# Performance work log

Measured on AMD Instinct MI355X. Metric: run time of the kernel, lower is better.

Reference implementation:

```python
import jax, jax.numpy as jnp
import numpy as np

B, N, D, E = 2, 50000, 128, 640000


def setup_inputs() -> dict:
    key = jax.random.key(0)
    ks = jax.random.split(key, 7)
    x = jax.random.normal(ks[0], (B, N, D), dtype=jnp.float32)
    edge_index = jax.random.randint(ks[1], (2, E), 0, N)
    edge_attr = jax.random.uniform(ks[2], (E,), dtype=jnp.float32)
    s = 1.0 / np.sqrt(D)
    W1 = jax.random.uniform(ks[3], (D, D), jnp.float32, -s, s)
    b1 = jax.random.uniform(ks[4], (D,), jnp.float32, -s, s)
    W2 = jax.random.uniform(ks[5], (D, D), jnp.float32, -s, s)
    b2 = jax.random.uniform(ks[6], (D,), jnp.float32, -s, s)
    return {"x": x, "edge_index": edge_index, "edge_attr": edge_attr,
            "W1": W1, "b1": b1, "W2": W2, "b2": b2}


def _gcn_layer(x, W, b, row, col, norm, n):
    # x: [B, N, D] -> transform then gather-scale-scatter along edges
    h = jnp.einsum('bnd,df->bnf', x, W)
    msg = h[:, row, :] * norm[None, :, None]          # [B, E2, D]
    agg = jax.vmap(lambda m: jax.ops.segment_sum(m, col, num_segments=n))(msg)
    return agg + b


def reference(x, edge_index, edge_attr, W1, b1, W2, b2):
    n = x.shape[1]
    row, col = edge_index[0], edge_index[1]
    # GCNConv default: add self loops (weight 1), symmetric normalization
    loop = jnp.arange(n)
    row2 = jnp.concatenate([row, loop])
    col2 = jnp.concatenate([col, loop])
    w2 = jnp.concatenate([edge_attr, jnp.ones((n,), edge_attr.dtype)])
    deg = jax.ops.segment_sum(w2, col2, num_segments=n)
    dinv = jnp.where(deg > 0, jax.lax.rsqrt(deg), 0.0)
    norm = dinv[row2] * w2 * dinv[col2]               # [E2]
    # dropout is identity in eval mode
    h = jax.nn.relu(_gcn_layer(x, W1, b1, row2, col2, norm, n))
    h = jax.nn.relu(_gcn_layer(h, W2, b2, row2, col2, norm, n))
    return h
```

## Files before the change

### kernel.cpp

```cpp
#include <hip/hip_runtime.h>

#define NNODES 50000
#define NBATCH 2
#define DIM    128
#define NEDGE  640000
#define M_TOT  (NBATCH*NNODES)
#define NXCD   8
#define NBL_N  196

typedef unsigned short u16;
typedef unsigned int   u32;
typedef unsigned long long u64;

typedef __attribute__((ext_vector_type(8))) short bf16x8;
typedef __attribute__((ext_vector_type(4))) float f32x4;

__device__ __forceinline__ float bf2f(u16 u){ return __uint_as_float(((u32)u)<<16); }
__device__ __forceinline__ u16 f2bf(float f){
    u32 x = __float_as_uint(f);
    x += 0x7fffu + ((x>>16)&1u);
    return (u16)(x>>16);
}

__global__ __launch_bounds__(256) void count_k(const int* __restrict__ ei,
                                               const float* __restrict__ ea,
                                               u64* __restrict__ part,
                                               u32* __restrict__ rankpack){
    u32 xcc = __builtin_amdgcn_s_getreg(6164) & 7u;
    int e = blockIdx.x*256 + threadIdx.x;
    if (e < NEDGE){
        int c = ei[NEDGE + e];
        u64 inc = (((u64)__float2uint_rn(ea[e] * 16777216.0f)) << 32) | 1ull;
        u64 old = __hip_atomic_fetch_add(&part[(size_t)xcc*NNODES + c], inc,
                                         __ATOMIC_RELAXED, __HIP_MEMORY_SCOPE_WORKGROUP);
        rankpack[e] = ((u32)old & 0xffffu) | (xcc << 16);
    }
}

__global__ __launch_bounds__(256) void scan1(const u64* __restrict__ part,
                                             int* __restrict__ cnt,
                                             int* __restrict__ poff,
                                             float* __restrict__ dinv,
                                             int* colstart, int* bsum){
    __shared__ int s[256];
    int tid = threadIdx.x;
    int n = blockIdx.x*256 + tid;
    int v = 0;
    if (n < NNODES){
        int run = 0; u64 fsum = 0;
        #pragma unroll
        for (int p = 0; p < NXCD; ++p){
            u64 pv = part[(size_t)p*NNODES + n];
            poff[p*NNODES + n] = run;
            run  += (int)(pv & 0xffffffffu);
            fsum += (pv >> 32);
        }
        cnt[n] = run;
        v = run;
        float deg = 1.0f + (float)fsum * (1.0f/16777216.0f);
        dinv[n] = rsqrtf(deg);
    }
    s[tid] = v; __syncthreads();
    #pragma unroll
    for (int off = 1; off < 256; off <<= 1){
        int t = (tid >= off) ? s[tid-off] : 0;
        __syncthreads();
        s[tid] += t;
        __syncthreads();
    }
    if (n < NNODES) colstart[n] = s[tid] - v;
    if (tid == 255) bsum[blockIdx.x] = s[255];
}

__global__ __launch_bounds__(256) void scan23(int* colstart, const int* __restrict__ bsum){
    __shared__ int s[256];
    int tid = threadIdx.x;
    int v = (tid < NBL_N) ? bsum[tid] : 0;
    s[tid] = v; __syncthreads();
    #pragma unroll
    for (int off = 1; off < 256; off <<= 1){
        int t = (tid >= off) ? s[tid-off] : 0;
        __syncthreads();
        s[tid] += t;
        __syncthreads();
    }
    int add = s[blockIdx.x] - bsum[blockIdx.x];
    int i = blockIdx.x*256 + tid;
    if (i < NNODES) colstart[i] += add;
}

__global__ __launch_bounds__(256) void fill_k(const int* __restrict__ ei,
                                              const float* __restrict__ ea,
                                              const float* __restrict__ dinv,
                                              const int* __restrict__ colstart,
                                              const int* __restrict__ poff,
                                              const u32* __restrict__ rankpack,
                                              int2* __restrict__ epack){
    int e = blockIdx.x*256 + threadIdx.x;
    if (e < NEDGE){
        int r = ei[e], c = ei[NEDGE + e];
        u32 rp = rankpack[e];
        int pos = colstart[c] + poff[(rp >> 16)*NNODES + c] + (int)(rp & 0xffffu);
        epack[pos] = make_int2(r, __float_as_int(dinv[r] * ea[e] * dinv[c]));
    }
}

__global__ __launch_bounds__(256) void transposeW(const float* __restrict__ W1, u16* __restrict__ Wt1,
                                                  const float* __restrict__ W2, u16* __restrict__ Wt2){
    int i = blockIdx.x*256 + threadIdx.x;
    const float* W = (i < 16384) ? W1 : W2;
    u16* Wt       = (i < 16384) ? Wt1 : Wt2;
    int ii = i & 16383;
    int k = ii >> 7, n = ii & 127;
    Wt[n*DIM + k] = f2bf(W[ii]);
}

__device__ __forceinline__ bf16x8 load_frag(const float* A, size_t off){
    const float4* ap = (const float4*)(A + off);
    float4 lo = ap[0], hi = ap[1];
    bf16x8 r;
    r[0] = (short)f2bf(lo.x); r[1] = (short)f2bf(lo.y);
    r[2] = (short)f2bf(lo.z); r[3] = (short)f2bf(lo.w);
    r[4] = (short)f2bf(hi.x); r[5] = (short)f2bf(hi.y);
    r[6] = (short)f2bf(hi.z); r[7] = (short)f2bf(hi.w);
    return r;
}
__device__ __forceinline__ bf16x8 load_frag(const u16* A, size_t off){
    return *(const bf16x8*)(A + off);
}

template <typename AT>
__global__ __launch_bounds__(256) void gemm128(const AT* __restrict__ A,
                                               const u16* __restrict__ Wt,
                                               u16* __restrict__ H, int M){
    __shared__ u16 Wl[128][136];
    int tid = threadIdx.x;
    {
        const uint4* src = (const uint4*)Wt;
        #pragma unroll
        for (int j = 0; j < 8; ++j){
            int g = tid + j*256;
            int n = g >> 4;
            int k = (g & 15) * 8;
            *(uint4*)&Wl[n][k] = src[g];
        }
    }
    __syncthreads();

    int wave = tid >> 6, lane = tid & 63;
    int quad = lane >> 4, r = lane & 15;
    int row0 = blockIdx.x*256 + wave*64;

    f32x4 acc[4][8];
    #pragma unroll
    for (int mt = 0; mt < 4; ++mt)
        #pragma unroll
        for (int nt = 0; nt < 8; ++nt)
            acc[mt][nt] = (f32x4){0.f,0.f,0.f,0.f};

    #pragma unroll
    for (int ks = 0; ks < 4; ++ks){
        bf16x8 af[4];
        #pragma unroll
        for (int mt = 0; mt < 4; ++mt){
            int row = row0 + mt*16 + r;
            if (row < M)
                af[mt] = load_frag(A, (size_t)row*DIM + ks*32 + quad*8);
            else
                af[mt] = (bf16x8){0,0,0,0,0,0,0,0};
        }
        #pragma unroll
        for (int nt = 0; nt < 8; ++nt){
            bf16x8 bfr = *(const bf16x8*)&Wl[nt*16 + r][ks*32 + quad*8];
            #pragma unroll
            for (int mt = 0; mt < 4; ++mt)
                acc[mt][nt] = __builtin_amdgcn_mfma_f32_16x16x32_bf16(af[mt], bfr, acc[mt][nt], 0, 0, 0);
        }
    }

    #pragma unroll
    for (int mt = 0; mt < 4; ++mt){
        #pragma unroll
        for (int reg = 0; reg < 4; ++reg){
            int row = row0 + mt*16 + quad*4 + reg;
            if (row < M){
                #pragma unroll
                for (int nt = 0; nt < 8; ++nt)
                    H[(size_t)row*DIM + nt*16 + r] = f2bf(acc[mt][nt][reg]);
            }
        }
    }
}

#define EFMA(W_, V_)                                        \
    a0 = fmaf(W_, bf2f((u16)((V_) & 0xffff)), a0);          \
    a1 = fmaf(W_, bf2f((u16)((V_) >> 16)),    a1);

template <bool OUT_F32>
__global__ __launch_bounds__(256) void gather1b_k(const u16* __restrict__ H,
                                                  const int2* __restrict__ epack,
                                                  const int* __restrict__ colstart,
                                                  const int* __restrict__ cnt,
                                                  const float* __restrict__ dinv,
                                                  const float* __restrict__ bias,
                                                  void* __restrict__ out){
    int wave = threadIdx.x >> 6, lane = threadIdx.x & 63;
    int bid = blockIdx.x;
    int batch = bid & 1;
    int n = (bid >> 1)*4 + wave;
    if (n >= NNODES) return;
    const u32* Hb = (const u32*)H + (size_t)batch*NNODES*64;

    float dn = dinv[n], dn2 = dn*dn;
    u32 sv = Hb[(size_t)n*64 + lane];
    float a0 = dn2*bf2f((u16)(sv & 0xffff));
    float a1 = dn2*bf2f((u16)(sv >> 16));

    int s = colstart[n], c = cnt[n];
    for (int base = 0; base < c; base += 64){
        int m = min(64, c - base);
        int2 ep = make_int2(0, 0);
        if (lane < m) ep = epack[s + base + lane];
        for (int j = 0; j < m; j += 8){
            int r0 = __shfl(ep.x, j+0), r1 = __shfl(ep.x, j+1);
            int r2 = __shfl(ep.x, j+2), r3 = __shfl(ep.x, j+3);
            int r4 = __shfl(ep.x, j+4), r5 = __shfl(ep.x, j+5);
            int r6 = __shfl(ep.x, j+6), r7 = __shfl(ep.x, j+7);
            float w0 = __int_as_float(__shfl(ep.y, j+0));
            float w1 = __int_as_float(__shfl(ep.y, j+1));
            float w2 = __int_as_float(__shfl(ep.y, j+2));
            float w3 = __int_as_float(__shfl(ep.y, j+3));
            float w4 = __int_as_float(__shfl(ep.y, j+4));
            float w5 = __int_as_float(__shfl(ep.y, j+5));
            float w6 = __int_as_float(__shfl(ep.y, j+6));
            float w7 = __int_as_float(__shfl(ep.y, j+7));
            u32 v0 = Hb[(size_t)r0*64 + lane];
            u32 v1 = Hb[(size_t)r1*64 + lane];
            u32 v2 = Hb[(size_t)r2*64 + lane];
            u32 v3 = Hb[(size_t)r3*64 + lane];
            u32 v4 = Hb[(size_t)r4*64 + lane];
            u32 v5 = Hb[(size_t)r5*64 + lane];
            u32 v6 = Hb[(size_t)r6*64 + lane];
            u32 v7 = Hb[(size_t)r7*64 + lane];
            EFMA(w0, v0) EFMA(w1, v1) EFMA(w2, v2) EFMA(w3, v3)
            EFMA(w4, v4) EFMA(w5, v5) EFMA(w6, v6) EFMA(w7, v7)
        }
    }
    a0 = fmaxf(a0 + bias[lane*2    ], 0.f);
    a1 = fmaxf(a1 + bias[lane*2 + 1], 0.f);
    if (OUT_F32){
        float2* O = (float2*)out;
        O[(size_t)(batch*NNODES + n)*64 + lane] = make_float2(a0, a1);
    } else {
        u32* O = (u32*)out;
        O[(size_t)(batch*NNODES + n)*64 + lane] = (u32)f2bf(a0) | ((u32)f2bf(a1) << 16);
    }
}

extern "C" void kernel_launch(void* const* d_in, const int* in_sizes, int n_in,
                              void* d_out, int out_size, void* d_ws, size_t ws_size,
                              hipStream_t stream){
    const float* x  = (const float*)d_in[0];
    const int*   ei = (const int*)  d_in[1];
    const float* ea = (const float*)d_in[2];
    const float* W1 = (const float*)d_in[3];
    const float* b1 = (const float*)d_in[4];
    const float* W2 = (const float*)d_in[5];
    const float* b2 = (const float*)d_in[6];

    char* p = (char*)d_ws;
    auto alloc = [&](size_t bytes)->char*{ char* r = p; p += (bytes + 511) & ~(size_t)511; return r; };
    u64*   part     = (u64*)  alloc((size_t)NXCD*NNODES*8);
    u32*   rankpack = (u32*)  alloc((size_t)NEDGE*4);
    int*   poff     = (int*)  alloc((size_t)NXCD*NNODES*4);
    float* dinv     = (float*)alloc(NNODES*4);
    int*   cnt      = (int*)  alloc(NNODES*4);
    int*   colstart = (int*)  alloc(NNODES*4);
    int*   bsum     = (int*)  alloc(1024);
    int2*  epack    = (int2*) alloc((size_t)NEDGE*8);
    u16*   Wt1      = (u16*)  alloc(DIM*DIM*2);
    u16*   Wt2      = (u16*)  alloc(DIM*DIM*2);
    u16*   h        = (u16*)  alloc((size_t)M_TOT*DIM*2);
    u16*   o1       = (u16*)  alloc((size_t)M_TOT*DIM*2);

    const int NBL_E = (NEDGE  + 255)/256;
    const int NTILE = (M_TOT + 255)/256;
    const int NBL_G = 2*((NNODES + 3)/4);

    hipMemsetAsync(part, 0, (size_t)NXCD*NNODES*8, stream);
    transposeW<<<128, 256, 0, stream>>>(W1, Wt1, W2, Wt2);
    count_k<<<NBL_E, 256, 0, stream>>>(ei, ea, part, rankpack);
    scan1  <<<NBL_N, 256, 0, stream>>>(part, cnt, poff, dinv, colstart, bsum);
    scan23 <<<NBL_N, 256, 0, stream>>>(colstart, bsum);
    fill_k <<<NBL_E, 256, 0, stream>>>(ei, ea, dinv, colstart, poff, rankpack, epack);

    gemm128<float><<<NTILE, 256, 0, stream>>>(x, Wt1, h, M_TOT);
    gather1b_k<false><<<NBL_G, 256, 0, stream>>>(h, epack, colstart, cnt, dinv, b1, o1);
    gemm128<u16>  <<<NTILE, 256, 0, stream>>>(o1, Wt2, h, M_TOT);
    gather1b_k<true> <<<NBL_G, 256, 0, stream>>>(h, epack, colstart, cnt, dinv, b2, d_out);
}
```

Before: 285.1 us.

## Fold block-offset scan into fill kernel and read edges via scalar loads in gather

Removes the scan23 launch by having every fill block redo the tiny scan of block sums in shared memory and add the block prefix to each edge's column start. The final column starts are written to a separate array, but only for nodes that have at least one edge; the gather skips reading that array when the count is zero. The gather kernel now makes the node's count and start wave-uniform and loads edge (row, weight) pairs directly from memory instead of loading 64 lanes and broadcasting with shuffles, aiming at scalar loads and fewer cross-lane ops. It also vectorises the bias load. The cost is redundant per-block scans and many duplicate writes of the same start value in fill.

After: 304.2 us. 6.7% more time.

```diff
diff --git a/kernel.cpp b/kernel.cpp
--- a/kernel.cpp
+++ b/kernel.cpp
@@ -72,8 +72,17 @@
     if (tid == 255) bsum[blockIdx.x] = s[255];
 }
 
-__global__ __launch_bounds__(256) void scan23(int* colstart, const int* __restrict__ bsum){
+__global__ __launch_bounds__(256) void fill_k(const int* __restrict__ ei,
+                                              const float* __restrict__ ea,
+                                              const float* __restrict__ dinv,
+                                              const int* __restrict__ colstart,
+                                              const int* __restrict__ bsum,
+                                              const int* __restrict__ poff,
+                                              const u32* __restrict__ rankpack,
+                                              int* __restrict__ colstartF,
+                                              int2* __restrict__ epack){
     __shared__ int s[256];
+    __shared__ int pre[256];
     int tid = threadIdx.x;
     int v = (tid < NBL_N) ? bsum[tid] : 0;
     s[tid] = v; __syncthreads();
@@ -84,23 +93,16 @@
         s[tid] += t;
         __syncthreads();
     }
-    int add = s[blockIdx.x] - bsum[blockIdx.x];
-    int i = blockIdx.x*256 + tid;
-    if (i < NNODES) colstart[i] += add;
-}
-
-__global__ __launch_bounds__(256) void fill_k(const int* __restrict__ ei,
-                                              const float* __restrict__ ea,
-                                              const float* __restrict__ dinv,
-                                              const int* __restrict__ colstart,
-                                              const int* __restrict__ poff,
-                                              const u32* __restrict__ rankpack,
-                                              int2* __restrict__ epack){
-    int e = blockIdx.x*256 + threadIdx.x;
+    pre[tid] = s[tid] - v;
+    __syncthreads();
+
+    int e = blockIdx.x*256 + tid;
     if (e < NEDGE){
         int r = ei[e], c = ei[NEDGE + e];
         u32 rp = rankpack[e];
-        int pos = colstart[c] + poff[(rp >> 16)*NNODES + c] + (int)(rp & 0xffffu);
+        int base = colstart[c] + pre[c >> 8];
+        colstartF[c] = base;
+        int pos = base + poff[(rp >> 16)*NNODES + c] + (int)(rp & 0xffffu);
         epack[pos] = make_int2(r, __float_as_int(dinv[r] * ea[e] * dinv[c]));
     }
 }
@@ -197,57 +199,58 @@
     a1 = fmaf(W_, bf2f((u16)((V_) >> 16)),    a1);
 
 template <bool OUT_F32>
-__global__ __launch_bounds__(256) void gather1b_k(const u16* __restrict__ H,
-                                                  const int2* __restrict__ epack,
-                                                  const int* __restrict__ colstart,
-                                                  const int* __restrict__ cnt,
-                                                  const float* __restrict__ dinv,
-                                                  const float* __restrict__ bias,
-                                                  void* __restrict__ out){
+__global__ __launch_bounds__(256) void gather3_k(const u16* __restrict__ H,
+                                                 const int2* __restrict__ epack,
+                                                 const int* __restrict__ colstartF,
+                                                 const int* __restrict__ cnt,
+                                                 const float* __restrict__ dinv,
+                                                 const float* __restrict__ bias,
+                                                 void* __restrict__ out){
     int wave = threadIdx.x >> 6, lane = threadIdx.x & 63;
-    int bid = blockIdx.x;
-    int batch = bid & 1;
-    int n = (bid >> 1)*4 + wave;
+    int batch = blockIdx.x & 1;
+    int n = (blockIdx.x >> 1)*4 + wave;
     if (n >= NNODES) return;
     const u32* Hb = (const u32*)H + (size_t)batch*NNODES*64;
+
+    int c = __builtin_amdgcn_readfirstlane(cnt[n]);
+    int s = (c > 0) ? __builtin_amdgcn_readfirstlane(colstartF[n]) : 0;
 
     float dn = dinv[n], dn2 = dn*dn;
     u32 sv = Hb[(size_t)n*64 + lane];
     float a0 = dn2*bf2f((u16)(sv & 0xffff));
     float a1 = dn2*bf2f((u16)(sv >> 16));
 
-    int s = colstart[n], c = cnt[n];
-    for (int base = 0; base < c; base += 64){
-        int m = min(64, c - base);
-        int2 ep = make_int2(0, 0);
-        if (lane < m) ep = epack[s + base + lane];
-        for (int j = 0; j < m; j += 8){
-            int r0 = __shfl(ep.x, j+0), r1 = __shfl(ep.x, j+1);
-            int r2 = __shfl(ep.x, j+2), r3 = __shfl(ep.x, j+3);
-            int r4 = __shfl(ep.x, j+4), r5 = __shfl(ep.x, j+5);
-            int r6 = __shfl(ep.x, j+6), r7 = __shfl(ep.x, j+7);
-            float w0 = __int_as_float(__shfl(ep.y, j+0));
-            float w1 = __int_as_float(__shfl(ep.y, j+1));
-            float w2 = __int_as_float(__shfl(ep.y, j+2));
-            float w3 = __int_as_float(__shfl(ep.y, j+3));
-            float w4 = __int_as_float(__shfl(ep.y, j+4));
-            float w5 = __int_as_float(__shfl(ep.y, j+5));
-            float w6 = __int_as_float(__shfl(ep.y, j+6));
-            float w7 = __int_as_float(__shfl(ep.y, j+7));
-            u32 v0 = Hb[(size_t)r0*64 + lane];
-            u32 v1 = Hb[(size_t)r1*64 + lane];
-            u32 v2 = Hb[(size_t)r2*64 + lane];
-            u32 v3 = Hb[(size_t)r3*64 + lane];
-            u32 v4 = Hb[(size_t)r4*64 + lane];
-            u32 v5 = Hb[(size_t)r5*64 + lane];
-            u32 v6 = Hb[(size_t)r6*64 + lane];
-            u32 v7 = Hb[(size_t)r7*64 + lane];
-            EFMA(w0, v0) EFMA(w1, v1) EFMA(w2, v2) EFMA(w3, v3)
-            EFMA(w4, v4) EFMA(w5, v5) EFMA(w6, v6) EFMA(w7, v7)
-        }
-    }
-    a0 = fmaxf(a0 + bias[lane*2    ], 0.f);
-    a1 = fmaxf(a1 + bias[lane*2 + 1], 0.f);
+    const int2* ep = epack + s;
+    int j = 0;
+    for (; j + 8 <= c; j += 8){
+        int2 e0 = ep[j+0], e1 = ep[j+1], e2 = ep[j+2], e3 = ep[j+3];
+        int2 e4 = ep[j+4], e5 = ep[j+5], e6 = ep[j+6], e7 = ep[j+7];
+        u32 v0 = Hb[(size_t)(u32)e0.x*64 + lane];
+        u32 v1 = Hb[(size_t)(u32)e1.x*64 + lane];
+        u32 v2 = Hb[(size_t)(u32)e2.x*64 + lane];
+        u32 v3 = Hb[(size_t)(u32)e3.x*64 + lane];
+        u32 v4 = Hb[(size_t)(u32)e4.x*64 + lane];
+        u32 v5 = Hb[(size_t)(u32)e5.x*64 + lane];
+        u32 v6 = Hb[(size_t)(u32)e6.x*64 + lane];
+        u32 v7 = Hb[(size_t)(u32)e7.x*64 + lane];
+        EFMA(__int_as_float(e0.y), v0)
+        EFMA(__int_as_float(e1.y), v1)
+        EFMA(__int_as_float(e2.y), v2)
+        EFMA(__int_as_float(e3.y), v3)
+        EFMA(__int_as_float(e4.y), v4)
+        EFMA(__int_as_float(e5.y), v5)
+        EFMA(__int_as_float(e6.y), v6)
+        EFMA(__int_as_float(e7.y), v7)
+    }
+    for (; j < c; ++j){
+        int2 e = ep[j];
+        u32 v = Hb[(size_t)(u32)e.x*64 + lane];
+        EFMA(__int_as_float(e.y), v)
+    }
+
+    float2 bb = ((const float2*)bias)[lane];
+    a0 = fmaxf(a0 + bb.x, 0.f);
+    a1 = fmaxf(a1 + bb.y, 0.f);
     if (OUT_F32){
         float2* O = (float2*)out;
         O[(size_t)(batch*NNODES + n)*64 + lane] = make_float2(a0, a1);
@@ -276,6 +279,7 @@
     float* dinv     = (float*)alloc(NNODES*4);
     int*   cnt      = (int*)  alloc(NNODES*4);
     int*   colstart = (int*)  alloc(NNODES*4);
+    int*   colstartF= (int*)  alloc(NNODES*4);
     int*   bsum     = (int*)  alloc(1024);
     int2*  epack    = (int2*) alloc((size_t)NEDGE*8);
     u16*   Wt1      = (u16*)  alloc(DIM*DIM*2);
@@ -291,11 +295,10 @@
     transposeW<<<128, 256, 0, stream>>>(W1, Wt1, W2, Wt2);
     count_k<<<NBL_E, 256, 0, stream>>>(ei, ea, part, rankpack);
     scan1  <<<NBL_N, 256, 0, stream>>>(part, cnt, poff, dinv, colstart, bsum);
-    scan23 <<<NBL_N, 256, 0, stream>>>(colstart, bsum);
-    fill_k <<<NBL_E, 256, 0, stream>>>(ei, ea, dinv, colstart, poff, rankpack, epack);
+    fill_k <<<NBL_E, 256, 0, stream>>>(ei, ea, dinv, colstart, bsum, poff, rankpack, colstartF, epack);
 
     gemm128<float><<<NTILE, 256, 0, stream>>>(x, Wt1, h, M_TOT);
-    gather1b_k<false><<<NBL_G, 256, 0, stream>>>(h, epack, colstart, cnt, dinv, b1, o1);
+    gather3_k<false><<<NBL_G, 256, 0, stream>>>(h, epack, colstartF, cnt, dinv, b1, o1);
     gemm128<u16>  <<<NTILE, 256, 0, stream>>>(o1, Wt2, h, M_TOT);
-    gather1b_k<true> <<<NBL_G, 256, 0, stream>>>(h, epack, colstart, cnt, dinv, b2, d_out);
-}
+    gather3_k<true> <<<NBL_G, 256, 0, stream>>>(h, epack, colstartF, cnt, dinv, b2, d_out);
+}
```
